# Performance work log

Hardware: AMD Instinct MI355X
Metric: run time of the kernel (lower is better)

## Reference

```python
import jax, jax.numpy as jnp
import numpy as np

B, T, C, K, D, N, ITERS = 16384, 8, 16, 4, 16, 16, 3


def setup_inputs() -> dict:
    key = jax.random.key(0)
    ks = jax.random.split(key, 12)
    rn = lambda k, s, sc=0.1: jax.random.normal(k, s, jnp.float32) * sc
    return {
        'frames': jax.random.uniform(ks[0], (B, T, 1, 16, 16), jnp.float32),
        'enc_w': rn(ks[1], (C, 1, 4, 4)), 'enc_b': jnp.zeros((C,), jnp.float32),
        'ln_w': jnp.ones((C,), jnp.float32), 'ln_b': jnp.zeros((C,), jnp.float32),
        'slot_mu': rn(ks[2], (1, K, D)),
        'wq': rn(ks[3], (D, D)), 'wk': rn(ks[4], (D, C)), 'wv': rn(ks[5], (D, C)),
        'gru_wih': rn(ks[6], (3 * D, D)), 'gru_whh': rn(ks[7], (3 * D, D)),
        'gru_bih': jnp.zeros((3 * D,), jnp.float32), 'gru_bhh': jnp.zeros((3 * D,), jnp.float32),
        's2s_w': rn(ks[8], (C * 16, D)), 's2s_b': jnp.zeros((C * 16,), jnp.float32),
        'mix_w': rn(ks[9], (C, K * C)), 'mix_b': jnp.zeros((C,), jnp.float32),
        'dec_w': rn(ks[10], (C, 1, 4, 4)), 'dec_b': jnp.zeros((1,), jnp.float32),
    }


def reference(frames, enc_w, enc_b, ln_w, ln_b, slot_mu, wq, wk, wv,
              gru_wih, gru_whh, gru_bih, gru_bhh, s2s_w, s2s_b,
              mix_w, mix_b, dec_w, dec_b):
    Bv, Tv = frames.shape[0], frames.shape[1]
    scale = D ** (-0.5)

    def layernorm(x):
        mu = jnp.mean(x, -1, keepdims=True)
        var = jnp.mean(jnp.square(x - mu), -1, keepdims=True)
        return (x - mu) * jax.lax.rsqrt(var + 1e-5) * ln_w + ln_b

    def gru_cell(x, h):  # torch GRUCell semantics, x,h: [M, D]
        gi = x @ gru_wih.T + gru_bih
        gh = h @ gru_whh.T + gru_bhh
        ir, iz, inn = jnp.split(gi, 3, axis=-1)
        hr, hz, hn = jnp.split(gh, 3, axis=-1)
        r = jax.nn.sigmoid(ir + hr)
        z = jax.nn.sigmoid(iz + hz)
        n = jnp.tanh(inn + r * hn)
        return (1.0 - z) * n + z * h

    def step(slots, frame):  # frame: [B,1,16,16]
        # encoder: conv k4 s4 -> [B,C,4,4], exact (erf) GELU as in torch default
        f = jax.lax.conv_general_dilated(frame, enc_w, (4, 4), 'VALID')
        f = jax.nn.gelu(f + enc_b[None, :, None, None], approximate=False)
        feat = f.reshape(Bv, C, N).transpose(0, 2, 1)  # [B,N,C]
        x = layernorm(feat)
        kk = x @ wk.T  # [B,N,D]
        vv = x @ wv.T
        s = slots
        for _ in range(ITERS):
            q = s @ wq.T                                  # [B,K,D]
            attn = jnp.einsum('bkd,bnd->bkn', q, kk) * scale
            attn = jax.nn.softmax(attn, axis=1)           # softmax over slots
            upd = jnp.einsum('bkn,bnd->bkd', attn, vv)
            s = gru_cell(upd.reshape(-1, D), s.reshape(-1, D)).reshape(Bv, K, D)
        spat = s @ s2s_w.T + s2s_b                        # [B,K,C*16]
        mixed = spat.reshape(Bv, K * C, 4, 4)
        mixed = jnp.einsum('oc,bchw->bohw', mix_w, mixed) + mix_b[None, :, None, None]
        # transposed conv k4 s4 (non-overlapping): each input pixel -> 4x4 block
        pred = jnp.einsum('bcij,code->boidje', mixed, dec_w).reshape(Bv, 1, 16, 16)
        pred = jax.nn.sigmoid(pred + dec_b[None, :, None, None])
        return s, pred

    slots0 = jnp.broadcast_to(slot_mu, (Bv, K, D))
    xs = jnp.swapaxes(frames[:, 1:Tv - 1], 0, 1)  # [T-2, B, 1, 16, 16]
    _, preds = jax.lax.scan(step, slots0, xs)
    return jnp.swapaxes(preds, 0, 1)  # [B, T-2, 1, 16, 16]
```

## Files before the change

### kernel.cpp

```cpp
#include <hip/hip_runtime.h>

#define TH 512
#define BPB 8

typedef float f32x2 __attribute__((ext_vector_type(2)));

__device__ __forceinline__ f32x2 mk2(float a, float b) { f32x2 r; r.x = a; r.y = b; return r; }
__device__ __forceinline__ f32x2 bc2(float a) { f32x2 r; r.x = a; r.y = a; return r; }
__device__ __forceinline__ f32x2 pkfma(f32x2 a, f32x2 b, f32x2 c) {
  asm("v_pk_fma_f32 %0, %1, %2, %3" : "=v"(c) : "v"(a), "v"(b), "0"(c));
  return c;
}

__device__ __forceinline__ float sigm(float x) {
  return __fdividef(1.0f, 1.0f + __expf(-x));
}
__device__ __forceinline__ float fast_tanh(float x) {
  float ex = __expf(2.0f * x);
  return 1.0f - __fdividef(2.0f, ex + 1.0f);
}

#define WAVE_SYNC() asm volatile("s_waitcnt lgkmcnt(0)" ::: "memory")

__device__ __forceinline__ float dot16b(const float* __restrict__ p, const f32x2* x, float bias) {
  const float4 w0 = *(const float4*)(p);
  const float4 w1 = *(const float4*)(p + 4);
  const float4 w2 = *(const float4*)(p + 8);
  const float4 w3 = *(const float4*)(p + 12);
  f32x2 a = mk2(bias, 0.f), b = mk2(0.f, 0.f);
  a = pkfma(mk2(w0.x, w0.y), x[0], a); b = pkfma(mk2(w0.z, w0.w), x[1], b);
  a = pkfma(mk2(w1.x, w1.y), x[2], a); b = pkfma(mk2(w1.z, w1.w), x[3], b);
  a = pkfma(mk2(w2.x, w2.y), x[4], a); b = pkfma(mk2(w2.z, w2.w), x[5], b);
  a = pkfma(mk2(w3.x, w3.y), x[6], a); b = pkfma(mk2(w3.z, w3.w), x[7], b);
  f32x2 s = a + b;
  return s.x + s.y;
}

__global__ void prep_kernel(const float* __restrict__ s2s_w, const float* __restrict__ s2s_b,
                            const float* __restrict__ mix_w, const float* __restrict__ mix_b,
                            const float* __restrict__ dec_w, const float* __restrict__ dec_b,
                            float* __restrict__ M2T, float* __restrict__ C0) {
  const int pix = threadIdx.x;
  const int I = pix >> 4, J = pix & 15;
  const int i = I >> 2, dd = I & 3, j = J >> 2, ee = J & 3;
  const int p = i*4 + j, q = dd*4 + ee;
  float DWrow[64];
  for (int kc = 0; kc < 64; ++kc) {
    float a = 0.f;
    for (int o = 0; o < 16; ++o) a += dec_w[o*16 + q] * mix_w[o*64 + kc];
    DWrow[kc] = a;
  }
  float c0 = dec_b[0];
  for (int o = 0; o < 16; ++o) c0 += dec_w[o*16 + q] * mix_b[o];
  for (int k = 0; k < 4; ++k)
    for (int c = 0; c < 16; ++c) c0 += DWrow[k*16 + c] * s2s_b[c*16 + p];
  C0[pix] = c0;
  for (int k = 0; k < 4; ++k)
    for (int d = 0; d < 16; ++d) {
      float a = 0.f;
      for (int c = 0; c < 16; ++c) a += DWrow[k*16 + c] * s2s_w[(c*16 + p)*16 + d];
      M2T[(k*16 + d)*256 + pix] = a;
    }
}

__launch_bounds__(TH, 8)
__global__ void microslot_kernel(
    const float* __restrict__ frames,
    const float* __restrict__ enc_w, const float* __restrict__ enc_b,
    const float* __restrict__ ln_w,  const float* __restrict__ ln_b,
    const float* __restrict__ slot_mu,
    const float* __restrict__ wq, const float* __restrict__ wk, const float* __restrict__ wv,
    const float* __restrict__ wih, const float* __restrict__ whh,
    const float* __restrict__ bih, const float* __restrict__ bhh,
    const float* __restrict__ g_M2T, const float* __restrict__ g_C0,
    float* __restrict__ out)
{
  __shared__ __align__(16) float W_enc[16*20];
  __shared__ __align__(16) float W_qT[16*20];
  __shared__ __align__(16) float W_k[16*20];
  __shared__ __align__(16) float W_v[16*20];
  __shared__ __align__(16) float W_ih[48*20];
  __shared__ __align__(16) float W_hh[48*20];
  __shared__ float B_enc[16], LNW[16], LNB[16], B_ih[48], B_hh[48], MU[64];
  __shared__ __align__(16) float C0L[256];
  __shared__ __align__(16) float svb[BPB*68];
  __shared__ __align__(16) float SCR[BPB][1088];

  const int tid = threadIdx.x;

  for (int idx = tid; idx < 256; idx += TH) W_enc[(idx>>4)*20 + (idx&15)] = enc_w[idx];
  for (int idx = tid; idx < 256; idx += TH) W_qT[(idx&15)*20 + (idx>>4)] = wq[idx];
  for (int idx = tid; idx < 256; idx += TH) W_k [(idx>>4)*20 + (idx&15)] = wk[idx];
  for (int idx = tid; idx < 256; idx += TH) W_v [(idx>>4)*20 + (idx&15)] = wv[idx];
  for (int idx = tid; idx < 768; idx += TH) W_ih[(idx>>4)*20 + (idx&15)] = wih[idx];
  for (int idx = tid; idx < 768; idx += TH) W_hh[(idx>>4)*20 + (idx&15)] = whh[idx];
  for (int idx = tid; idx < 256; idx += TH) C0L[idx] = g_C0[idx];
  if (tid < 16) { B_enc[tid] = enc_b[tid]; LNW[tid] = ln_w[tid]; LNB[tid] = ln_b[tid]; }
  if (tid >= 64  && tid < 112) B_ih[tid-64]  = bih[tid-64];
  if (tid >= 128 && tid < 176) B_hh[tid-128] = bhh[tid-128];
  if (tid >= 448) MU[tid-448] = slot_mu[tid-448];
  __syncthreads();

  const int wid = tid >> 6, lane = tid & 63;
  const int ln = lane & 15, lg = lane >> 4;
  float* S = SCR[wid];
  constexpr int o_sb = 0, o_tmp = 64, o_xq = 128, o_kk = 448, o_vv = 768;

  float s_reg = MU[lane];
  const int i0 = ln >> 2, j0 = ln & 3;
  const size_t fbase = (size_t)(blockIdx.x * BPB + wid) * (8*256);

  for (int st = 0; st < 6; ++st) {
    const int t = st + 1;
    f32x2 patch2[8];
    {
      const float* fp = frames + fbase + (size_t)t*256;
      #pragma unroll
      for (int a = 0; a < 4; ++a) {
        float4 pv = *(const float4*)(fp + (4*i0 + a)*16 + 4*j0);
        patch2[2*a]   = mk2(pv.x, pv.y);
        patch2[2*a+1] = mk2(pv.z, pv.w);
      }
    }
    float x4[4];
    #pragma unroll
    for (int cc = 0; cc < 4; ++cc) {
      int c = 4*lg + cc;
      float acc = dot16b(&W_enc[c*20], patch2, B_enc[c]);
      x4[cc] = 0.5f * acc * (1.0f + erff(acc * 0.70710678118654752440f));
    }
    float s1 = x4[0]+x4[1]+x4[2]+x4[3];
    float s2 = x4[0]*x4[0]+x4[1]*x4[1]+x4[2]*x4[2]+x4[3]*x4[3];
    s1 += __shfl_xor(s1, 16); s1 += __shfl_xor(s1, 32);
    s2 += __shfl_xor(s2, 16); s2 += __shfl_xor(s2, 32);
    float mu  = s1 * 0.0625f;
    float var = s2 * 0.0625f - mu*mu;
    float rs  = rsqrtf(var + 1e-5f);
    #pragma unroll
    for (int cc = 0; cc < 4; ++cc) {
      int c = 4*lg + cc;
      x4[cc] = (x4[cc]-mu)*rs*LNW[c] + LNB[c];
    }
    *(float4*)&S[o_xq + ln*20 + 4*lg] = make_float4(x4[0],x4[1],x4[2],x4[3]);
    WAVE_SYNC();

    {
      f32x2 xr2[8];
      #pragma unroll
      for (int qd = 0; qd < 4; ++qd) {
        float4 v = *(const float4*)&S[o_xq + ln*20 + 4*qd];
        xr2[2*qd]   = mk2(v.x, v.y);
        xr2[2*qd+1] = mk2(v.z, v.w);
      }
      float kk4[4];
      #pragma unroll
      for (int cc = 0; cc < 4; ++cc) {
        int dd = 4*lg + cc;
        kk4[cc] = dot16b(&W_k[dd*20], xr2, 0.f);
        S[o_vv + dd*20 + ln] = dot16b(&W_v[dd*20], xr2, 0.f);
      }
      *(float4*)&S[o_kk + ln*20 + 4*lg] = make_float4(kk4[0],kk4[1],kk4[2],kk4[3]);
    }
    WAVE_SYNC();
    {
      f32x2 kkr2[8];
      #pragma unroll
      for (int qd = 0; qd < 4; ++qd) {
        float4 v = *(const float4*)&S[o_kk + ln*20 + 4*qd];
        kkr2[2*qd]   = mk2(v.x, v.y);
        kkr2[2*qd+1] = mk2(v.z, v.w);
      }
      float kq4[4];
      #pragma unroll
      for (int cc = 0; cc < 4; ++cc)
        kq4[cc] = dot16b(&W_qT[(4*lg+cc)*20], kkr2, 0.f);
      *(float4*)&S[o_xq + ln*20 + 4*lg] = make_float4(kq4[0],kq4[1],kq4[2],kq4[3]);
    }

    for (int it = 0; it < 3; ++it) {
      S[o_sb + lane] = s_reg;
      WAVE_SYNC();
      f32x2 hr2[8];
      #pragma unroll
      for (int qd = 0; qd < 4; ++qd) {
        float4 v = *(const float4*)&S[o_sb + lg*16 + 4*qd];
        hr2[2*qd]   = mk2(v.x, v.y);
        hr2[2*qd+1] = mk2(v.z, v.w);
      }
      float l = 0.25f * dot16b(&S[o_xq + ln*20], hr2, 0.f);
      float m = fmaxf(l, __shfl_xor(l, 16)); m = fmaxf(m, __shfl_xor(m, 32));
      float e = __expf(l - m);
      float se = e + __shfl_xor(e, 16); se += __shfl_xor(se, 32);
      S[o_tmp + lane] = __fdividef(e, se);
      WAVE_SYNC();
      f32x2 ar2[4], vr2[4];
      #pragma unroll
      for (int qd = 0; qd < 2; ++qd) {
        float4 a = *(const float4*)&S[o_tmp + lg*16 + 8*qd];
        float4 a2 = *(const float4*)&S[o_tmp + lg*16 + 8*qd + 4];
        float4 v = *(const float4*)&S[o_vv + ln*20 + 8*qd];
        float4 v2 = *(const float4*)&S[o_vv + ln*20 + 8*qd + 4];
        ar2[2*qd] = mk2(a.x,a.y); ar2[2*qd+1] = mk2(a2.x,a2.y);
        vr2[2*qd] = mk2(v.x,v.y); vr2[2*qd+1] = mk2(v2.x,v2.y);
        (void)a; (void)v;
      }
      float u;
      {
        float4 a0 = *(const float4*)&S[o_tmp + lg*16];
        float4 a1 = *(const float4*)&S[o_tmp + lg*16 + 4];
        float4 a2 = *(const float4*)&S[o_tmp + lg*16 + 8];
        float4 a3 = *(const float4*)&S[o_tmp + lg*16 + 12];
        float4 v0 = *(const float4*)&S[o_vv + ln*20];
        float4 v1 = *(const float4*)&S[o_vv + ln*20 + 4];
        float4 v2 = *(const float4*)&S[o_vv + ln*20 + 8];
        float4 v3 = *(const float4*)&S[o_vv + ln*20 + 12];
        f32x2 pa = mk2(0.f,0.f), pb = mk2(0.f,0.f);
        pa = pkfma(mk2(a0.x,a0.y), mk2(v0.x,v0.y), pa);
        pb = pkfma(mk2(a0.z,a0.w), mk2(v0.z,v0.w), pb);
        pa = pkfma(mk2(a1.x,a1.y), mk2(v1.x,v1.y), pa);
        pb = pkfma(mk2(a1.z,a1.w), mk2(v1.z,v1.w), pb);
        pa = pkfma(mk2(a2.x,a2.y), mk2(v2.x,v2.y), pa);
        pb = pkfma(mk2(a2.z,a2.w), mk2(v2.z,v2.w), pb);
        pa = pkfma(mk2(a3.x,a3.y), mk2(v3.x,v3.y), pa);
        pb = pkfma(mk2(a3.z,a3.w), mk2(v3.z,v3.w), pb);
        f32x2 ps = pa + pb;
        u = ps.x + ps.y;
      }
      S[o_tmp + lane] = u;
      WAVE_SYNC();
      f32x2 ur2[8];
      #pragma unroll
      for (int qd = 0; qd < 4; ++qd) {
        float4 v = *(const float4*)&S[o_tmp + lg*16 + 4*qd];
        ur2[2*qd]   = mk2(v.x, v.y);
        ur2[2*qd+1] = mk2(v.z, v.w);
      }
      f32x2 gir2 = mk2(B_ih[ln],    0.f), ghr2 = mk2(B_hh[ln],    0.f);
      f32x2 giz2 = mk2(B_ih[16+ln], 0.f), ghz2 = mk2(B_hh[16+ln], 0.f);
      f32x2 gin2 = mk2(B_ih[32+ln], 0.f), ghn2 = mk2(B_hh[32+ln], 0.f);
      #pragma unroll
      for (int qd = 0; qd < 4; ++qd) {
        float4 wr = *(const float4*)&W_ih[(   ln)*20 + 4*qd];
        float4 wz = *(const float4*)&W_ih[(16+ln)*20 + 4*qd];
        float4 wn = *(const float4*)&W_ih[(32+ln)*20 + 4*qd];
        float4 vr = *(const float4*)&W_hh[(   ln)*20 + 4*qd];
        float4 vz = *(const float4*)&W_hh[(16+ln)*20 + 4*qd];
        float4 vn = *(const float4*)&W_hh[(32+ln)*20 + 4*qd];
        gir2 = pkfma(mk2(wr.x,wr.y), ur2[2*qd], gir2); gir2 = pkfma(mk2(wr.z,wr.w), ur2[2*qd+1], gir2);
        giz2 = pkfma(mk2(wz.x,wz.y), ur2[2*qd], giz2); giz2 = pkfma(mk2(wz.z,wz.w), ur2[2*qd+1], giz2);
        gin2 = pkfma(mk2(wn.x,wn.y), ur2[2*qd], gin2); gin2 = pkfma(mk2(wn.z,wn.w), ur2[2*qd+1], gin2);
        ghr2 = pkfma(mk2(vr.x,vr.y), hr2[2*qd], ghr2); ghr2 = pkfma(mk2(vr.z,vr.w), hr2[2*qd+1], ghr2);
        ghz2 = pkfma(mk2(vz.x,vz.y), hr2[2*qd], ghz2); ghz2 = pkfma(mk2(vz.z,vz.w), hr2[2*qd+1], ghz2);
        ghn2 = pkfma(mk2(vn.x,vn.y), hr2[2*qd], ghn2); ghn2 = pkfma(mk2(vn.z,vn.w), hr2[2*qd+1], ghn2);
      }
      float rg = sigm((gir2.x+gir2.y) + (ghr2.x+ghr2.y));
      float zg = sigm((giz2.x+giz2.y) + (ghz2.x+ghz2.y));
      float nh = fast_tanh((gin2.x+gin2.y) + rg*(ghn2.x+ghn2.y));
      s_reg = (1.f - zg)*nh + zg*s_reg;
    }

    svb[wid*68 + lane] = s_reg;
    __syncthreads();
    {
      const int u = lane & 7, r = lane >> 3;
      const int pix = (wid << 5) | (u << 2);
      const float* m2p = g_M2T + pix;
      float4 c0 = *(const float4*)&C0L[pix];
      f32x2 a01 = mk2(c0.x, c0.y), a23 = mk2(c0.z, c0.w);
      #pragma unroll 4
      for (int q4 = 0; q4 < 16; ++q4) {
        float4 sv = *(const float4*)&svb[r*68 + 4*q4];
        float4 m0 = *(const float4*)(m2p + (4*q4+0)*256);
        float4 m1 = *(const float4*)(m2p + (4*q4+1)*256);
        float4 m2 = *(const float4*)(m2p + (4*q4+2)*256);
        float4 m3 = *(const float4*)(m2p + (4*q4+3)*256);
        a01 = pkfma(mk2(m0.x,m0.y), bc2(sv.x), a01); a23 = pkfma(mk2(m0.z,m0.w), bc2(sv.x), a23);
        a01 = pkfma(mk2(m1.x,m1.y), bc2(sv.y), a01); a23 = pkfma(mk2(m1.z,m1.w), bc2(sv.y), a23);
        a01 = pkfma(mk2(m2.x,m2.y), bc2(sv.z), a01); a23 = pkfma(mk2(m2.z,m2.w), bc2(sv.z), a23);
        a01 = pkfma(mk2(m3.x,m3.y), bc2(sv.w), a01); a23 = pkfma(mk2(m3.z,m3.w), bc2(sv.w), a23);
      }
      const size_t ob = (size_t)(blockIdx.x*BPB + r)*(6*256) + (size_t)st*256 + pix;
      *(float4*)(out + ob) = make_float4(sigm(a01.x), sigm(a01.y), sigm(a23.x), sigm(a23.y));
    }
    __syncthreads();
  }
}

extern "C" void kernel_launch(void* const* d_in, const int* in_sizes, int n_in,
                              void* d_out, int out_size, void* d_ws, size_t ws_size,
                              hipStream_t stream) {
  const float* frames  = (const float*)d_in[0];
  const float* enc_w   = (const float*)d_in[1];
  const float* enc_b   = (const float*)d_in[2];
  const float* ln_w    = (const float*)d_in[3];
  const float* ln_b    = (const float*)d_in[4];
  const float* slot_mu = (const float*)d_in[5];
  const float* wq      = (const float*)d_in[6];
  const float* wk      = (const float*)d_in[7];
  const float* wv      = (const float*)d_in[8];
  const float* wih     = (const float*)d_in[9];
  const float* whh     = (const float*)d_in[10];
  const float* bih     = (const float*)d_in[11];
  const float* bhh     = (const float*)d_in[12];
  const float* s2s_w   = (const float*)d_in[13];
  const float* s2s_b   = (const float*)d_in[14];
  const float* mix_w   = (const float*)d_in[15];
  const float* mix_b   = (const float*)d_in[16];
  const float* dec_w   = (const float*)d_in[17];
  const float* dec_b   = (const float*)d_in[18];
  float* out = (float*)d_out;

  float* g_M2T = (float*)d_ws;
  float* g_C0  = g_M2T + 64*256;

  hipLaunchKernelGGL(prep_kernel, dim3(1), dim3(256), 0, stream,
                     s2s_w, s2s_b, mix_w, mix_b, dec_w, dec_b, g_M2T, g_C0);

  const int B = 16384;
  hipLaunchKernelGGL(microslot_kernel, dim3(B / BPB), dim3(TH), 0, stream,
                     frames, enc_w, enc_b, ln_w, ln_b, slot_mu, wq, wk, wv,
                     wih, whh, bih, bhh, g_M2T, g_C0, out);
}
```

Measured before the change: 348.2 us.

## Trim per-step ALU work: polynomial GELU, drop softmax max, cache V in registers

Replaces erff with an Abramowitz-Stegun polynomial GELU and removes the max-subtraction from the slot softmax. It keeps the value vectors in registers across the three attention iterations, loads the GRU biases and C0 directly into registers or from global memory instead of staging them in LDS, and uses op_sel packed FMAs to avoid broadcast moves. It also lowers the launch-bounds occupancy hint from 8 to 6. Dropping the max makes the softmax vulnerable to overflow on large logits, and the polynomial erf approximation adds small numerical error.

```diff
diff --git a/kernel.cpp b/kernel.cpp
--- a/kernel.cpp
+++ b/kernel.cpp
@@ -6,11 +6,18 @@
 typedef float f32x2 __attribute__((ext_vector_type(2)));
 
 __device__ __forceinline__ f32x2 mk2(float a, float b) { f32x2 r; r.x = a; r.y = b; return r; }
-__device__ __forceinline__ f32x2 bc2(float a) { f32x2 r; r.x = a; r.y = a; return r; }
 __device__ __forceinline__ f32x2 pkfma(f32x2 a, f32x2 b, f32x2 c) {
   asm("v_pk_fma_f32 %0, %1, %2, %3" : "=v"(c) : "v"(a), "v"(b), "0"(c));
   return c;
 }
+__device__ __forceinline__ f32x2 pkfma_blo(f32x2 a, f32x2 b, f32x2 c) {
+  asm("v_pk_fma_f32 %0, %1, %2, %3 op_sel_hi:[1,0,1]" : "=v"(c) : "v"(a), "v"(b), "0"(c));
+  return c;
+}
+__device__ __forceinline__ f32x2 pkfma_bhi(f32x2 a, f32x2 b, f32x2 c) {
+  asm("v_pk_fma_f32 %0, %1, %2, %3 op_sel:[0,1,0] op_sel_hi:[1,1,1]" : "=v"(c) : "v"(a), "v"(b), "0"(c));
+  return c;
+}
 
 __device__ __forceinline__ float sigm(float x) {
   return __fdividef(1.0f, 1.0f + __expf(-x));
@@ -18,6 +25,18 @@
 __device__ __forceinline__ float fast_tanh(float x) {
   float ex = __expf(2.0f * x);
   return 1.0f - __fdividef(2.0f, ex + 1.0f);
+}
+__device__ __forceinline__ float gelu_erf(float a) {
+  float z = fabsf(a) * 0.70710678118654752440f;
+  float t = __fdividef(1.0f, __builtin_fmaf(0.3275911f, z, 1.0f));
+  float p = __builtin_fmaf(1.061405429f, t, -1.453152027f);
+  p = __builtin_fmaf(p, t, 1.421413741f);
+  p = __builtin_fmaf(p, t, -0.284496736f);
+  p = __builtin_fmaf(p, t, 0.254829592f);
+  p = p * t;
+  float e = __expf(-z * z);
+  float y = __builtin_fmaf(-p, e, 1.0f);
+  return 0.5f * a * (1.0f + copysignf(y, a));
 }
 
 #define WAVE_SYNC() asm volatile("s_waitcnt lgkmcnt(0)" ::: "memory")
@@ -63,7 +82,7 @@
     }
 }
 
-__launch_bounds__(TH, 8)
+__launch_bounds__(TH, 6)
 __global__ void microslot_kernel(
     const float* __restrict__ frames,
     const float* __restrict__ enc_w, const float* __restrict__ enc_b,
@@ -81,8 +100,7 @@
   __shared__ __align__(16) float W_v[16*20];
   __shared__ __align__(16) float W_ih[48*20];
   __shared__ __align__(16) float W_hh[48*20];
-  __shared__ float B_enc[16], LNW[16], LNB[16], B_ih[48], B_hh[48], MU[64];
-  __shared__ __align__(16) float C0L[256];
+  __shared__ float B_enc[16], LNW[16], LNB[16];
   __shared__ __align__(16) float svb[BPB*68];
   __shared__ __align__(16) float SCR[BPB][1088];
 
@@ -94,11 +112,7 @@
   for (int idx = tid; idx < 256; idx += TH) W_v [(idx>>4)*20 + (idx&15)] = wv[idx];
   for (int idx = tid; idx < 768; idx += TH) W_ih[(idx>>4)*20 + (idx&15)] = wih[idx];
   for (int idx = tid; idx < 768; idx += TH) W_hh[(idx>>4)*20 + (idx&15)] = whh[idx];
-  for (int idx = tid; idx < 256; idx += TH) C0L[idx] = g_C0[idx];
   if (tid < 16) { B_enc[tid] = enc_b[tid]; LNW[tid] = ln_w[tid]; LNB[tid] = ln_b[tid]; }
-  if (tid >= 64  && tid < 112) B_ih[tid-64]  = bih[tid-64];
-  if (tid >= 128 && tid < 176) B_hh[tid-128] = bhh[tid-128];
-  if (tid >= 448) MU[tid-448] = slot_mu[tid-448];
   __syncthreads();
 
   const int wid = tid >> 6, lane = tid & 63;
@@ -106,7 +120,10 @@
   float* S = SCR[wid];
   constexpr int o_sb = 0, o_tmp = 64, o_xq = 128, o_kk = 448, o_vv = 768;
 
-  float s_reg = MU[lane];
+  float s_reg = slot_mu[lane];
+  const float bi_r = bih[ln], bi_z = bih[16+ln], bi_n = bih[32+ln];
+  const float bh_r = bhh[ln], bh_z = bhh[16+ln], bh_n = bhh[32+ln];
+
   const int i0 = ln >> 2, j0 = ln & 3;
   const size_t fbase = (size_t)(blockIdx.x * BPB + wid) * (8*256);
 
@@ -127,7 +144,7 @@
     for (int cc = 0; cc < 4; ++cc) {
       int c = 4*lg + cc;
       float acc = dot16b(&W_enc[c*20], patch2, B_enc[c]);
-      x4[cc] = 0.5f * acc * (1.0f + erff(acc * 0.70710678118654752440f));
+      x4[cc] = gelu_erf(acc);
     }
     float s1 = x4[0]+x4[1]+x4[2]+x4[3];
     float s2 = x4[0]*x4[0]+x4[1]*x4[1]+x4[2]*x4[2]+x4[3]*x4[3];
@@ -162,6 +179,8 @@
       *(float4*)&S[o_kk + ln*20 + 4*lg] = make_float4(kk4[0],kk4[1],kk4[2],kk4[3]);
     }
     WAVE_SYNC();
+
+    f32x2 vvr[8];
     {
       f32x2 kkr2[8];
       #pragma unroll
@@ -169,6 +188,9 @@
         float4 v = *(const float4*)&S[o_kk + ln*20 + 4*qd];
         kkr2[2*qd]   = mk2(v.x, v.y);
         kkr2[2*qd+1] = mk2(v.z, v.w);
+        float4 w = *(const float4*)&S[o_vv + ln*20 + 4*qd];
+        vvr[2*qd]   = mk2(w.x, w.y);
+        vvr[2*qd+1] = mk2(w.z, w.w);
       }
       float kq4[4];
       #pragma unroll
@@ -188,41 +210,25 @@
         hr2[2*qd+1] = mk2(v.z, v.w);
       }
       float l = 0.25f * dot16b(&S[o_xq + ln*20], hr2, 0.f);
-      float m = fmaxf(l, __shfl_xor(l, 16)); m = fmaxf(m, __shfl_xor(m, 32));
-      float e = __expf(l - m);
+      float e = __expf(l);
       float se = e + __shfl_xor(e, 16); se += __shfl_xor(se, 32);
       S[o_tmp + lane] = __fdividef(e, se);
       WAVE_SYNC();
-      f32x2 ar2[4], vr2[4];
-      #pragma unroll
-      for (int qd = 0; qd < 2; ++qd) {
-        float4 a = *(const float4*)&S[o_tmp + lg*16 + 8*qd];
-        float4 a2 = *(const float4*)&S[o_tmp + lg*16 + 8*qd + 4];
-        float4 v = *(const float4*)&S[o_vv + ln*20 + 8*qd];
-        float4 v2 = *(const float4*)&S[o_vv + ln*20 + 8*qd + 4];
-        ar2[2*qd] = mk2(a.x,a.y); ar2[2*qd+1] = mk2(a2.x,a2.y);
-        vr2[2*qd] = mk2(v.x,v.y); vr2[2*qd+1] = mk2(v2.x,v2.y);
-        (void)a; (void)v;
-      }
       float u;
       {
         float4 a0 = *(const float4*)&S[o_tmp + lg*16];
         float4 a1 = *(const float4*)&S[o_tmp + lg*16 + 4];
         float4 a2 = *(const float4*)&S[o_tmp + lg*16 + 8];
         float4 a3 = *(const float4*)&S[o_tmp + lg*16 + 12];
-        float4 v0 = *(const float4*)&S[o_vv + ln*20];
-        float4 v1 = *(const float4*)&S[o_vv + ln*20 + 4];
-        float4 v2 = *(const float4*)&S[o_vv + ln*20 + 8];
-        float4 v3 = *(const float4*)&S[o_vv + ln*20 + 12];
         f32x2 pa = mk2(0.f,0.f), pb = mk2(0.f,0.f);
-        pa = pkfma(mk2(a0.x,a0.y), mk2(v0.x,v0.y), pa);
-        pb = pkfma(mk2(a0.z,a0.w), mk2(v0.z,v0.w), pb);
-        pa = pkfma(mk2(a1.x,a1.y), mk2(v1.x,v1.y), pa);
-        pb = pkfma(mk2(a1.z,a1.w), mk2(v1.z,v1.w), pb);
-        pa = pkfma(mk2(a2.x,a2.y), mk2(v2.x,v2.y), pa);
-        pb = pkfma(mk2(a2.z,a2.w), mk2(v2.z,v2.w), pb);
-        pa = pkfma(mk2(a3.x,a3.y), mk2(v3.x,v3.y), pa);
-        pb = pkfma(mk2(a3.z,a3.w), mk2(v3.z,v3.w), pb);
+        pa = pkfma(mk2(a0.x,a0.y), vvr[0], pa);
+        pb = pkfma(mk2(a0.z,a0.w), vvr[1], pb);
+        pa = pkfma(mk2(a1.x,a1.y), vvr[2], pa);
+        pb = pkfma(mk2(a1.z,a1.w), vvr[3], pb);
+        pa = pkfma(mk2(a2.x,a2.y), vvr[4], pa);
+        pb = pkfma(mk2(a2.z,a2.w), vvr[5], pb);
+        pa = pkfma(mk2(a3.x,a3.y), vvr[6], pa);
+        pb = pkfma(mk2(a3.z,a3.w), vvr[7], pb);
         f32x2 ps = pa + pb;
         u = ps.x + ps.y;
       }
@@ -235,9 +241,9 @@
         ur2[2*qd]   = mk2(v.x, v.y);
         ur2[2*qd+1] = mk2(v.z, v.w);
       }
-      f32x2 gir2 = mk2(B_ih[ln],    0.f), ghr2 = mk2(B_hh[ln],    0.f);
-      f32x2 giz2 = mk2(B_ih[16+ln], 0.f), ghz2 = mk2(B_hh[16+ln], 0.f);
-      f32x2 gin2 = mk2(B_ih[32+ln], 0.f), ghn2 = mk2(B_hh[32+ln], 0.f);
+      f32x2 gir2 = mk2(bi_r, 0.f), ghr2 = mk2(bh_r, 0.f);
+      f32x2 giz2 = mk2(bi_z, 0.f), ghz2 = mk2(bh_z, 0.f);
+      f32x2 gin2 = mk2(bi_n, 0.f), ghn2 = mk2(bh_n, 0.f);
       #pragma unroll
       for (int qd = 0; qd < 4; ++qd) {
         float4 wr = *(const float4*)&W_ih[(   ln)*20 + 4*qd];
@@ -265,19 +271,20 @@
       const int u = lane & 7, r = lane >> 3;
       const int pix = (wid << 5) | (u << 2);
       const float* m2p = g_M2T + pix;
-      float4 c0 = *(const float4*)&C0L[pix];
+      float4 c0 = *(const float4*)(g_C0 + pix);
       f32x2 a01 = mk2(c0.x, c0.y), a23 = mk2(c0.z, c0.w);
       #pragma unroll 4
       for (int q4 = 0; q4 < 16; ++q4) {
         float4 sv = *(const float4*)&svb[r*68 + 4*q4];
+        f32x2 svA = mk2(sv.x, sv.y), svB = mk2(sv.z, sv.w);
         float4 m0 = *(const float4*)(m2p + (4*q4+0)*256);
         float4 m1 = *(const float4*)(m2p + (4*q4+1)*256);
         float4 m2 = *(const float4*)(m2p + (4*q4+2)*256);
         float4 m3 = *(const float4*)(m2p + (4*q4+3)*256);
-        a01 = pkfma(mk2(m0.x,m0.y), bc2(sv.x), a01); a23 = pkfma(mk2(m0.z,m0.w), bc2(sv.x), a23);
-        a01 = pkfma(mk2(m1.x,m1.y), bc2(sv.y), a01); a23 = pkfma(mk2(m1.z,m1.w), bc2(sv.y), a23);
-        a01 = pkfma(mk2(m2.x,m2.y), bc2(sv.z), a01); a23 = pkfma(mk2(m2.z,m2.w), bc2(sv.z), a23);
-        a01 = pkfma(mk2(m3.x,m3.y), bc2(sv.w), a01); a23 = pkfma(mk2(m3.z,m3.w), bc2(sv.w), a23);
+        a01 = pkfma_blo(mk2(m0.x,m0.y), svA, a01); a23 = pkfma_blo(mk2(m0.z,m0.w), svA, a23);
+        a01 = pkfma_bhi(mk2(m1.x,m1.y), svA, a01); a23 = pkfma_bhi(mk2(m1.z,m1.w), svA, a23);
+        a01 = pkfma_blo(mk2(m2.x,m2.y), svB, a01); a23 = pkfma_blo(mk2(m2.z,m2.w), svB, a23);
+        a01 = pkfma_bhi(mk2(m3.x,m3.y), svB, a01); a23 = pkfma_bhi(mk2(m3.z,m3.w), svB, a23);
       }
       const size_t ob = (size_t)(blockIdx.x*BPB + r)*(6*256) + (size_t)st*256 + pix;
       *(float4*)(out + ob) = make_float4(sigm(a01.x), sigm(a01.y), sigm(a23.x), sigm(a23.y));
```

After: 439.4 us. +26.2%, slower.
